# Performance work log

Hardware: AMD Instinct MI355X
Metric: run time of the kernel (lower is better)

## Reference

```python
import jax, jax.numpy as jnp
import numpy as np

E4M3_MAX = 448.0
IGNORE = -1000.0
ROTARY_BASE = 10000.0


def quant_dequant_e4m3(w):
    """Emulate per-tensor FP8 E4M3 quantize->dequantize (3 mantissa bits, max 448)."""
    amax = jnp.max(jnp.abs(w))
    scale = E4M3_MAX / jnp.maximum(amax, 1e-12)
    v = w * scale
    a = jnp.abs(v)
    # exponent clipped to E4M3 range (min normal exp -6, max 8)
    e = jnp.clip(jnp.floor(jnp.log2(jnp.maximum(a, 1e-30))), -6.0, 8.0)
    step = jnp.exp2(e - 3.0)  # 3 mantissa bits
    q = jnp.clip(jnp.round(v / step) * step, -E4M3_MAX, E4M3_MAX)
    return (q / scale).astype(w.dtype)


def rotary_sin_cos(rotary_dim, n_ctx):
    pos = jnp.arange(n_ctx, dtype=jnp.float32)
    dim = jnp.arange(rotary_dim // 2, dtype=jnp.float32)
    inv_freq = ROTARY_BASE ** (-dim / (rotary_dim / 2))
    ang = pos[:, None] * inv_freq[None, :]            # [n_ctx, rotary_dim//2]
    ang = jnp.concatenate([ang, ang], axis=-1)        # [n_ctx, rotary_dim]
    return jnp.sin(ang), jnp.cos(ang)


def apply_rotary(x, sin, cos, rotary_dim):
    # x: [B, S, H, Dh]; rotate first rotary_dim dims with rotate-half convention
    S = x.shape[1]
    x_rot, x_pass = x[..., :rotary_dim], x[..., rotary_dim:]
    half = rotary_dim // 2
    x_flip = jnp.concatenate([-x_rot[..., half:], x_rot[..., :half]], axis=-1)
    c = cos[:S][None, :, None, :]
    s = sin[:S][None, :, None, :]
    out = x_rot * c + x_flip * s
    return jnp.concatenate([out, x_pass], axis=-1) if rotary_dim < x.shape[-1] else out


def setup_inputs() -> dict:
    key = jax.random.key(0)
    ks = jax.random.split(key, 8)
    B, S, D, H, Dh = 2, 2048, 1024, 16, 64
    return {
        "query_input": jax.random.normal(ks[0], (B, S, D), jnp.float32),
        "key_input": jax.random.normal(ks[1], (B, S, D), jnp.float32),
        "value_input": jax.random.normal(ks[2], (B, S, D), jnp.float32),
        "W_Q": jax.random.normal(ks[3], (H, D, Dh), jnp.float32) * 0.02,
        "W_K": jax.random.normal(ks[4], (H, D, Dh), jnp.float32) * 0.02,
        "W_V": jax.random.normal(ks[5], (H, D, Dh), jnp.float32) * 0.02,
        "W_O": jax.random.normal(ks[6], (H, Dh, D), jnp.float32) * 0.02,
        "b_Q": jnp.zeros((H, Dh), jnp.float32),
        "b_K": jnp.zeros((H, Dh), jnp.float32),
        "b_V": jnp.zeros((H, Dh), jnp.float32),
        "b_O": jnp.zeros((D,), jnp.float32),
    }


def reference(query_input, key_input, value_input, W_Q, W_K, W_V, W_O, b_Q, b_K, b_V, b_O):
    B, S, D = query_input.shape
    H, _, Dh = W_Q.shape
    rotary_dim = Dh
    attn_scale = jnp.sqrt(jnp.asarray(Dh, jnp.float32))

    # FP8-quantized QKV weights/biases (E4M3 quant-dequant emulation)
    Wq = quant_dequant_e4m3(W_Q)
    Wk = quant_dequant_e4m3(W_K)
    Wv = quant_dequant_e4m3(W_V)
    bq = quant_dequant_e4m3(b_Q)
    bk = quant_dequant_e4m3(b_K)
    bv = quant_dequant_e4m3(b_V)

    q = jnp.einsum("bsd,hde->bshe", query_input, Wq) + bq  # [B,S,H,Dh]
    k = jnp.einsum("bsd,hde->bshe", key_input, Wk) + bk
    v = jnp.einsum("bsd,hde->bshe", value_input, Wv) + bv

    sin, cos = rotary_sin_cos(rotary_dim, S)
    q = apply_rotary(q, sin, cos, rotary_dim)
    k = apply_rotary(k, sin, cos, rotary_dim)

    scores = jnp.einsum("bqhe,bkhe->bhqk", q, k) / attn_scale  # [B,H,S,S]
    causal = jnp.tril(jnp.ones((S, S), bool))
    scores = jnp.where(causal[None, None], scores, IGNORE)
    pattern = jax.nn.softmax(scores, axis=-1)

    z = jnp.einsum("bhqk,bkhe->bqhe", pattern, v)             # [B,S,H,Dh]
    out = jnp.einsum("bqhe,hed->bqd", z, W_O) + b_O           # [B,S,D]
    return out
```

## Files before the change

### kernel.cpp

```cpp
#include <hip/hip_runtime.h>
#include <math.h>


typedef __attribute__((ext_vector_type(8))) short bf16x8;
typedef __attribute__((ext_vector_type(16))) float f32x16;
typedef __attribute__((ext_vector_type(4))) float f32x4;
typedef __attribute__((ext_vector_type(4))) float f4;

#define E4M3_MAX 448.0f

__device__ inline float bf2f(ushort u) { return __uint_as_float(((unsigned)u) << 16); }
__device__ inline ushort f2bf(float f) {
  unsigned u = __float_as_uint(f);
  return (ushort)((u + 0x7FFF + ((u >> 16) & 1)) >> 16);
}
__device__ inline unsigned pack2bf(float a, float b) {
  unsigned ua = __float_as_uint(a), ub = __float_as_uint(b);
  return ((ua + 0x8000u) >> 16) | ((ub + 0x8000u) & 0xFFFF0000u);
}

__device__ __forceinline__ void gll16(const ushort* g, ushort* l) {
  __builtin_amdgcn_global_load_lds(
      (const __attribute__((address_space(1))) unsigned int*)g,
      (__attribute__((address_space(3))) unsigned int*)l, 16, 0, 0);
}

__global__ void zero16_kernel(float* p) {
  if (threadIdx.x < 16) p[threadIdx.x] = 0.0f;
}

__global__ __launch_bounds__(256) void amax6_kernel(const float* __restrict__ p0,
                                                    const float* __restrict__ p1,
                                                    const float* __restrict__ p2,
                                                    const float* __restrict__ p3,
                                                    const float* __restrict__ p4,
                                                    const float* __restrict__ p5,
                                                    float* __restrict__ amax) {
  int y = blockIdx.y;
  const float* src = (y == 0) ? p0 : (y == 1) ? p1 : (y == 2) ? p2 : (y == 3) ? p3 : (y == 4) ? p4 : p5;
  int n = (y < 3) ? 1048576 : 1024;
  float m = 0.0f;
  int stride = gridDim.x * 256;
  for (int i = blockIdx.x * 256 + threadIdx.x; i < n; i += stride)
    m = fmaxf(m, fabsf(src[i]));
  #pragma unroll
  for (int off = 32; off > 0; off >>= 1)
    m = fmaxf(m, __shfl_xor(m, off));
  __shared__ float wred[4];
  if ((threadIdx.x & 63) == 0) wred[threadIdx.x >> 6] = m;
  __syncthreads();
  if (threadIdx.x == 0) {
    m = fmaxf(fmaxf(wred[0], wred[1]), fmaxf(wred[2], wred[3]));
    atomicMax((unsigned int*)(amax + y), __float_as_uint(m));
  }
}

__device__ inline float qdq_qval(float w, float amax) {
  float scale = E4M3_MAX / fmaxf(amax, 1e-12f);
  float v = w * scale;
  float a = fmaxf(fabsf(v), 1e-30f);
  int ex;
  (void)frexpf(a, &ex);
  float e = fminf(fmaxf((float)(ex - 1), -6.0f), 8.0f);
  float step = exp2f(e - 3.0f);
  float q = rintf(v / step) * step;
  return fminf(fmaxf(q, -E4M3_MAX), E4M3_MAX);
}

__global__ void qvec3_kernel(const float* __restrict__ b0, const float* __restrict__ b1,
                             const float* __restrict__ b2, const float* __restrict__ amax,
                             float* __restrict__ o0, float* __restrict__ o1,
                             float* __restrict__ o2) {
  int y = blockIdx.y;
  const float* b = (y == 0) ? b0 : (y == 1) ? b1 : b2;
  float* o = (y == 0) ? o0 : (y == 1) ? o1 : o2;
  float am = amax[3 + y];
  int idx = blockIdx.x * blockDim.x + threadIdx.x;
  if (idx < 1024) {
    float q = qdq_qval(b[idx], am);
    o[idx] = q * (fmaxf(am, 1e-12f) * (1.0f / E4M3_MAX));
  }
}

__global__ __launch_bounds__(256) void quant_repack_bt3(const float* __restrict__ W0,
                                                        const float* __restrict__ W1,
                                                        const float* __restrict__ W2,
                                                        const float* __restrict__ amaxp,
                                                        ushort* __restrict__ o0,
                                                        ushort* __restrict__ o1,
                                                        ushort* __restrict__ o2) {
  int z = blockIdx.z;
  const float* W = (z == 0) ? W0 : (z == 1) ? W1 : W2;
  ushort* Bt = (z == 0) ? o0 : (z == 1) ? o1 : o2;
  float amax = amaxp[z];
  __shared__ float tile[64][65];
  int d0 = blockIdx.x * 64, hh = blockIdx.y;
  int tid = threadIdx.x;
  int e = tid & 63, dd = tid >> 6;
  #pragma unroll
  for (int p = 0; p < 16; p++)
    tile[dd + p * 4][e] = W[(size_t)hh * 65536 + (size_t)(d0 + dd + p * 4) * 64 + e];
  __syncthreads();
  int d = tid & 63, ee = tid >> 6;
  #pragma unroll
  for (int p = 0; p < 16; p++) {
    int e2 = ee + p * 4;
    Bt[(size_t)(hh * 64 + e2) * 1024 + d0 + d] = f2bf(qdq_qval(tile[d][e2], amax));
  }
}

__global__ __launch_bounds__(256) void wo_trans(const float* __restrict__ W,
                                               ushort* __restrict__ Bt) {
  __shared__ float tile[64][65];
  int d0 = blockIdx.x * 64, he0 = blockIdx.y * 64;
  int tid = threadIdx.x;
  int dcol = tid & 63, hr = tid >> 6;
  #pragma unroll
  for (int p = 0; p < 16; p++)
    tile[hr + p * 4][dcol] = W[(size_t)(he0 + hr + p * 4) * 1024 + d0 + dcol];
  __syncthreads();
  int hcol = tid & 63, dr = tid >> 6;
  #pragma unroll
  for (int p = 0; p < 16; p++)
    Bt[(size_t)(d0 + dr + p * 4) * 1024 + he0 + hcol] = f2bf(tile[hcol][dr + p * 4]);
}

__global__ __launch_bounds__(256) void cvt3_kernel(const float* __restrict__ i0,
                                                   const float* __restrict__ i1,
                                                   const float* __restrict__ i2,
                                                   ushort* __restrict__ o0,
                                                   ushort* __restrict__ o1,
                                                   ushort* __restrict__ o2) {
  int y = blockIdx.y;
  const float* in = (y == 0) ? i0 : (y == 1) ? i1 : i2;
  ushort* out = (y == 0) ? o0 : (y == 1) ? o1 : o2;
  int i = blockIdx.x * 256 + threadIdx.x;
  f4 v = *(const f4*)(in + (size_t)i * 4);
  uint2 o;
  o.x = (unsigned)f2bf(v[0]) | ((unsigned)f2bf(v[1]) << 16);
  o.y = (unsigned)f2bf(v[2]) | ((unsigned)f2bf(v[3]) << 16);
  *(uint2*)(out + (size_t)i * 4) = o;
}

template <int QUANT, int TN>
__device__ __forceinline__ void gemm_body(const ushort* __restrict__ A,
                                          const ushort* __restrict__ Bt,
                                          const float* __restrict__ bias, float s_inv,
                                          ushort* __restrict__ outb, float* __restrict__ outf,
                                          int bx, int by, ushort* As, ushort* Bs) {
  const int K = 1024, N = 1024;
  const int JF = TN / 32;
  int tid = threadIdx.x;
  int w = tid >> 6, lane = tid & 63, quad = lane >> 4, l16 = lane & 15;
  int wm = w & 1, wn = w >> 1;
  int row0 = by * 128, col0 = bx * TN;
  f32x4 acc[4][4] = {};

  for (int k0 = 0; k0 < K; k0 += 32) {
    __syncthreads();
    {
      int u = tid;
      gll16(&A[(size_t)(row0 + (u >> 2)) * K + k0 + (u & 3) * 8], &As[u * 8]);
      u = tid + 256;
      gll16(&A[(size_t)(row0 + (u >> 2)) * K + k0 + (u & 3) * 8], &As[u * 8]);
      u = tid;
      gll16(&Bt[(size_t)(col0 + (u >> 2)) * K + k0 + (u & 3) * 8], &Bs[u * 8]);
      if (TN == 128) {
        u = tid + 256;
        gll16(&Bt[(size_t)(col0 + (u >> 2)) * K + k0 + (u & 3) * 8], &Bs[u * 8]);
      }
    }
    __syncthreads();
    bf16x8 af[4], bfr[JF];
    #pragma unroll
    for (int i = 0; i < 4; i++)
      af[i] = *(const bf16x8*)&As[(wm * 64 + i * 16 + l16) * 32 + quad * 8];
    #pragma unroll
    for (int j = 0; j < JF; j++)
      bfr[j] = *(const bf16x8*)&Bs[(wn * (TN / 2) + j * 16 + l16) * 32 + quad * 8];
    #pragma unroll
    for (int i = 0; i < 4; i++)
      #pragma unroll
      for (int j = 0; j < JF; j++)
        acc[i][j] = __builtin_amdgcn_mfma_f32_16x16x32_bf16(af[i], bfr[j], acc[i][j], 0, 0, 0);
  }

  #pragma unroll
  for (int j = 0; j < JF; j++) {
    int col = col0 + wn * (TN / 2) + j * 16 + l16;
    float bv = bias[col];
    #pragma unroll
    for (int i = 0; i < 4; i++) {
      int row = row0 + wm * 64 + i * 16 + quad * 4;
      #pragma unroll
      for (int r = 0; r < 4; r++) {
        float v = acc[i][j][r] * s_inv + bv;
        if (QUANT) outb[(size_t)(row + r) * N + col] = f2bf(v);
        else       outf[(size_t)(row + r) * N + col] = v;
      }
    }
  }
}

__global__ __launch_bounds__(256) void gemm3_qkv(const ushort* __restrict__ xq,
                                                 const ushort* __restrict__ xk,
                                                 const ushort* __restrict__ xv,
                                                 const ushort* __restrict__ wq,
                                                 const ushort* __restrict__ wk,
                                                 const ushort* __restrict__ wv,
                                                 const float* __restrict__ bq,
                                                 const float* __restrict__ bk,
                                                 const float* __restrict__ bv,
                                                 const float* __restrict__ amax,
                                                 ushort* __restrict__ oq,
                                                 ushort* __restrict__ ok,
                                                 ushort* __restrict__ ov) {
  __shared__ ushort As[4096], Bs[4096];
  int z = blockIdx.z;
  const ushort* A  = (z == 0) ? xq : (z == 1) ? xk : xv;
  const ushort* Bt = (z == 0) ? wq : (z == 1) ? wk : wv;
  const float* bias = (z == 0) ? bq : (z == 1) ? bk : bv;
  ushort* out = (z == 0) ? oq : (z == 1) ? ok : ov;
  float s_inv = fmaxf(amax[z], 1e-12f) * (1.0f / E4M3_MAX);
  gemm_body<1, 128>(A, Bt, bias, s_inv, out, nullptr, blockIdx.x, blockIdx.y, As, Bs);
}

__global__ __launch_bounds__(256) void gemm_wo(const ushort* __restrict__ A,
                                               const ushort* __restrict__ Bt,
                                               const float* __restrict__ bias,
                                               float* __restrict__ out) {
  __shared__ ushort As[4096], Bs[2048];
  gemm_body<0, 64>(A, Bt, bias, 1.0f, nullptr, out, blockIdx.x, blockIdx.y, As, Bs);
}

__global__ __launch_bounds__(256) void rotary_bf(ushort* qb, ushort* kb) {
  int bs = blockIdx.x;
  int s = bs & 2047;
  int tid = threadIdx.x;
  int e = tid & 63, w = tid >> 6;
  int j = e & 31;
  float inv_freq = exp2f((float)j * (-13.287712379549449f / 32.0f));
  float ang = (float)s * inv_freq;
  float c = cosf(ang), sn = sinf(ang);
  float sgn = (e < 32) ? -1.0f : 1.0f;
  size_t base = (size_t)bs * 1024;
  #pragma unroll
  for (int i = 0; i < 4; i++) {
    int h = w + i * 4;
    size_t idx = base + (size_t)h * 64 + e;
    float x = bf2f(qb[idx]);
    float xp = __shfl_xor(x, 32);
    qb[idx] = f2bf(x * c + sgn * xp * sn);
    float y = bf2f(kb[idx]);
    float yp = __shfl_xor(y, 32);
    kb[idx] = f2bf(y * c + sgn * yp * sn);
  }
}

__global__ __launch_bounds__(256) void v_trans(const ushort* __restrict__ v,
                                              ushort* __restrict__ vT) {
  __shared__ ushort tile[64][72];
  int s0 = blockIdx.x * 64, h = blockIdx.y, b = blockIdx.z;
  int tid = threadIdx.x;
  int e = tid & 63, sr = tid >> 6;
  #pragma unroll
  for (int p = 0; p < 16; p++)
    tile[sr + p * 4][e] = v[(size_t)(b * 2048 + s0 + sr + p * 4) * 1024 + h * 64 + e];
  __syncthreads();
  int sc = tid & 63, er = tid >> 6;
  #pragma unroll
  for (int p = 0; p < 16; p++)
    vT[(size_t)((b * 16 + h) * 64 + er + p * 4) * 2048 + s0 + sc] = tile[sc][er + p * 4];
}

__global__ __launch_bounds__(256, 2) void flash_mfma4(const ushort* __restrict__ qb,
                                                      const ushort* __restrict__ kb,
                                                      const ushort* __restrict__ vT,
                                                      ushort* __restrict__ zb) {
  int qt = (int)gridDim.x - 1 - (int)blockIdx.x;
  int h = blockIdx.y, b = blockIdx.z;
  int tid = threadIdx.x;
  int w = tid >> 6, lane = tid & 63, h2 = lane >> 5, l31 = lane & 31;
  __shared__ ushort sbuf[8192 + 9216];
  ushort* Ks = sbuf;
  ushort* Vs = sbuf + 4096;
  ushort* P2 = sbuf + 8192;

  const int q0 = qt * 128;
  const int qg = q0 + w * 32 + l31;
  const int qrow = w * 32 + l31;
  size_t qbase = ((size_t)(b * 2048 + qg)) * 1024 + (size_t)h * 64;
  bf16x8 qf[4];
  #pragma unroll
  for (int ck = 0; ck < 4; ck++)
    qf[ck] = *(const bf16x8*)&qb[qbase + ck * 16 + h2 * 8];

  f32x16 accO[2] = {};
  float mrun = -INFINITY, lrun = 0.0f;
  const float CE = 0.125f;

  const int u0 = tid, u1 = tid + 256;
  const int r0 = u0 >> 3, c0 = u0 & 7, r1 = u1 >> 3, c1 = u1 & 7;
  const int sw0 = (c0 ^ (r0 & 7)) * 8, sw1 = (c1 ^ (r1 & 7)) * 8;
  const ushort* ksrc0 = kb + ((size_t)(b * 2048 + r0)) * 1024 + (size_t)h * 64 + c0 * 8;
  const ushort* ksrc1 = kb + ((size_t)(b * 2048 + r1)) * 1024 + (size_t)h * 64 + c1 * 8;
  const ushort* vsrc0 = vT + ((size_t)((b * 16 + h) * 64 + r0)) * 2048 + c0 * 8;
  const ushort* vsrc1 = vT + ((size_t)((b * 16 + h) * 64 + r1)) * 2048 + c1 * 8;

  int ktmax = 2 * qt + 1;
  uint4 kc0 = *(const uint4*)ksrc0;
  uint4 kc1 = *(const uint4*)ksrc1;
  uint4 vc0 = *(const uint4*)vsrc0;
  uint4 vc1 = *(const uint4*)vsrc1;

  for (int kt = 0; kt <= ktmax; kt++) {
    __syncthreads();
    *(uint4*)&Ks[r0 * 64 + sw0] = kc0;
    *(uint4*)&Ks[r1 * 64 + sw1] = kc1;
    *(uint4*)&Vs[r0 * 64 + sw0] = vc0;
    *(uint4*)&Vs[r1 * 64 + sw1] = vc1;
    __syncthreads();
    if (kt < ktmax) {
      kc0 = *(const uint4*)(ksrc0 + (size_t)(kt + 1) * 65536);
      kc1 = *(const uint4*)(ksrc1 + (size_t)(kt + 1) * 65536);
      vc0 = *(const uint4*)(vsrc0 + (kt + 1) * 64);
      vc1 = *(const uint4*)(vsrc1 + (kt + 1) * 64);
    }

    bool active = (kt * 64 <= q0 + w * 32 + 31);
    if (active) {
      f32x16 sc[2] = {};
      #pragma unroll
      for (int mf = 0; mf < 2; mf++) {
        int row = mf * 32 + l31;
        int s8 = row & 7;
        #pragma unroll
        for (int ck = 0; ck < 4; ck++) {
          bf16x8 ka = *(const bf16x8*)&Ks[row * 64 + (((2 * ck + h2) ^ s8) * 8)];
          sc[mf] = __builtin_amdgcn_mfma_f32_32x32x16_bf16(ka, qf[ck], sc[mf], 0, 0, 0);
        }
      }

      if (kt * 64 + 63 > q0 + w * 32) {
        #pragma unroll
        for (int mf = 0; mf < 2; mf++)
          #pragma unroll
          for (int i = 0; i < 16; i++) {
            int kv = kt * 64 + mf * 32 + (i & 3) + 8 * (i >> 2) + 4 * h2;
            sc[mf][i] = (kv > qg) ? -8000.0f : sc[mf][i];
          }
      }

      float tm = sc[0][0];
      #pragma unroll
      for (int i = 1; i < 16; i++) tm = fmaxf(tm, sc[0][i]);
      #pragma unroll
      for (int i = 0; i < 16; i++) tm = fmaxf(tm, sc[1][i]);
      tm = fmaxf(tm, __shfl_xor(tm, 32));
      float mnew = fmaxf(mrun, tm);
      float alpha = __expf((mrun - mnew) * CE);
      float p[2][16];
      float rs = 0.0f;
      #pragma unroll
      for (int mf = 0; mf < 2; mf++)
        #pragma unroll
        for (int i = 0; i < 16; i++) {
          float pv = __expf((sc[mf][i] - mnew) * CE);
          p[mf][i] = pv;
          rs += pv;
        }
      rs += __shfl_xor(rs, 32);
      lrun = lrun * alpha + rs;
      mrun = mnew;
      #pragma unroll
      for (int mf = 0; mf < 2; mf++)
        #pragma unroll
        for (int i = 0; i < 16; i++) accO[mf][i] *= alpha;

      #pragma unroll
      for (int mf = 0; mf < 2; mf++)
        #pragma unroll
        for (int m = 0; m < 4; m++) {
          uint2 w2;
          w2.x = pack2bf(p[mf][4 * m + 0], p[mf][4 * m + 1]);
          w2.y = pack2bf(p[mf][4 * m + 2], p[mf][4 * m + 3]);
          *(uint2*)&P2[qrow * 72 + 32 * mf + 8 * m + 4 * h2] = w2;
        }
    }
    __syncthreads();
    if (active) {
      #pragma unroll
      for (int ck = 0; ck < 4; ck++) {
        bf16x8 pB = *(const bf16x8*)&P2[qrow * 72 + ck * 16 + h2 * 8];
        #pragma unroll
        for (int mf = 0; mf < 2; mf++) {
          int row = mf * 32 + l31;
          bf16x8 va = *(const bf16x8*)&Vs[row * 64 + (((2 * ck + h2) ^ (row & 7)) * 8)];
          accO[mf] = __builtin_amdgcn_mfma_f32_32x32x16_bf16(va, pB, accO[mf], 0, 0, 0);
        }
      }
    }
  }

  float inv = 1.0f / lrun;
  __syncthreads();
  ushort* Osb = P2;
  #pragma unroll
  for (int mf = 0; mf < 2; mf++)
    #pragma unroll
    for (int m = 0; m < 4; m++) {
      int e0 = 32 * mf + 8 * m + 4 * h2;
      float a0 = accO[mf][4 * m + 0] * inv, a1 = accO[mf][4 * m + 1] * inv;
      float a2 = accO[mf][4 * m + 2] * inv, a3 = accO[mf][4 * m + 3] * inv;
      *(unsigned*)&Osb[qrow * 72 + e0] = pack2bf(a0, a1);
      *(unsigned*)&Osb[qrow * 72 + e0 + 2] = pack2bf(a2, a3);
    }
  __syncthreads();
  size_t obase = ((size_t)(b * 2048 + q0)) * 1024 + (size_t)h * 64;
  #pragma unroll
  for (int i = 0; i < 4; i++) {
    int u = tid + i * 256;
    int r = u >> 3, blk = u & 7;
    *(uint4*)&zb[obase + (size_t)r * 1024 + blk * 8] = *(const uint4*)&Osb[r * 72 + blk * 8];
  }
}

extern "C" void kernel_launch(void* const* d_in, const int* in_sizes, int n_in,
                              void* d_out, int out_size, void* d_ws, size_t ws_size,
                              hipStream_t stream) {
  const float* Xq  = (const float*)d_in[0];
  const float* Xk  = (const float*)d_in[1];
  const float* Xv  = (const float*)d_in[2];
  const float* W_Q = (const float*)d_in[3];
  const float* W_K = (const float*)d_in[4];
  const float* W_V = (const float*)d_in[5];
  const float* W_O = (const float*)d_in[6];
  const float* b_Q = (const float*)d_in[7];
  const float* b_K = (const float*)d_in[8];
  const float* b_V = (const float*)d_in[9];
  const float* b_O = (const float*)d_in[10];
  float* out = (float*)d_out;

  char* base = (char*)d_ws;
  float*  amax = (float*)(base + 0);
  float*  bq   = (float*)(base + 4096);
  float*  bk   = (float*)(base + 8192);
  float*  bv   = (float*)(base + 12288);
  ushort* wq   = (ushort*)(base + 16384);
  ushort* wk   = (ushort*)(base + 16384 + 2097152);
  ushort* wv   = (ushort*)(base + 16384 + 2u * 2097152);
  ushort* woT  = (ushort*)(base + 16384 + 3u * 2097152);
  ushort* xq   = (ushort*)(base + 8404992);
  ushort* xk   = (ushort*)(base + 16793600);
  ushort* xv   = (ushort*)(base + 25182208);
  ushort* qbf  = (ushort*)(base + 33570816);
  ushort* kbf  = (ushort*)(base + 41959424);
  ushort* vbf  = (ushort*)(base + 50348032);
  ushort* vT   = xq;
  ushort* zbf  = xk;

  zero16_kernel<<<1, 64, 0, stream>>>(amax);
  dim3 agrid(64, 6);
  amax6_kernel<<<agrid, 256, 0, stream>>>(W_Q, W_K, W_V, b_Q, b_K, b_V, amax);

  dim3 rgrid(16, 16, 3);
  quant_repack_bt3<<<rgrid, 256, 0, stream>>>(W_Q, W_K, W_V, amax, wq, wk, wv);
  dim3 qvgrid(4, 3);
  qvec3_kernel<<<qvgrid, 256, 0, stream>>>(b_Q, b_K, b_V, amax, bq, bk, bv);
  dim3 wgrid(16, 16);
  wo_trans<<<wgrid, 256, 0, stream>>>(W_O, woT);
  dim3 cgrid(4096, 3);
  cvt3_kernel<<<cgrid, 256, 0, stream>>>(Xq, Xk, Xv, xq, xk, xv);

  dim3 g3(8, 32, 3);
  gemm3_qkv<<<g3, 256, 0, stream>>>(xq, xk, xv, wq, wk, wv, bq, bk, bv, amax,
                                    qbf, kbf, vbf);

  rotary_bf<<<4096, 256, 0, stream>>>(qbf, kbf);

  dim3 vgrid(32, 16, 2);
  v_trans<<<vgrid, 256, 0, stream>>>(vbf, vT);

  dim3 fgrid(16, 16, 2);
  flash_mfma4<<<fgrid, 256, 0, stream>>>(qbf, kbf, vT, zbf);

  dim3 wog(16, 32);
  gemm_wo<<<wog, 256, 0, stream>>>(zbf, woT, b_O, out);
}
```

Measured before the change: 275.1 us.

## Split flash attention KV range across two wave groups with final merge

The flash attention kernel now runs 512 threads per block. Two groups of four waves each take half of the causal key range for the same 128-query tile, and the partial outputs plus running max and sum are merged through shared memory at the end. The barrier between the P write and the PV matmul is also dropped, since each wave reads only its own P rows. This adds parallelism per query tile and shortens the serial KV loop, at the cost of doubled LDS use, a merge step and possible occupancy limits.

```diff
diff --git a/kernel.cpp b/kernel.cpp
--- a/kernel.cpp
+++ b/kernel.cpp
@@ -273,18 +273,21 @@
     vT[(size_t)((b * 16 + h) * 64 + er + p * 4) * 2048 + s0 + sc] = tile[sc][er + p * 4];
 }
 
-__global__ __launch_bounds__(256, 2) void flash_mfma4(const ushort* __restrict__ qb,
+__global__ __launch_bounds__(512, 4) void flash_mfma5(const ushort* __restrict__ qb,
                                                       const ushort* __restrict__ kb,
                                                       const ushort* __restrict__ vT,
                                                       ushort* __restrict__ zb) {
   int qt = (int)gridDim.x - 1 - (int)blockIdx.x;
   int h = blockIdx.y, b = blockIdx.z;
   int tid = threadIdx.x;
-  int w = tid >> 6, lane = tid & 63, h2 = lane >> 5, l31 = lane & 31;
-  __shared__ ushort sbuf[8192 + 9216];
-  ushort* Ks = sbuf;
-  ushort* Vs = sbuf + 4096;
-  ushort* P2 = sbuf + 8192;
+  int w8 = tid >> 6;
+  int g = w8 >> 2;
+  int w = w8 & 3;
+  int lane = tid & 63, h2 = lane >> 5, l31 = lane & 31;
+  __shared__ ushort sbuf[16384 + 18432];
+  ushort* Ks = sbuf + g * 4096;
+  ushort* Vs = sbuf + 8192 + g * 4096;
+  ushort* P2 = sbuf + 16384 + g * 9216;
 
   const int q0 = qt * 128;
   const int qg = q0 + w * 32 + l31;
@@ -299,32 +302,36 @@
   float mrun = -INFINITY, lrun = 0.0f;
   const float CE = 0.125f;
 
-  const int u0 = tid, u1 = tid + 256;
+  const int nt = qt + 1;
+  const int kt0 = g * nt;
+
+  const int ts = tid & 255;
+  const int u0 = ts, u1 = ts + 256;
   const int r0 = u0 >> 3, c0 = u0 & 7, r1 = u1 >> 3, c1 = u1 & 7;
   const int sw0 = (c0 ^ (r0 & 7)) * 8, sw1 = (c1 ^ (r1 & 7)) * 8;
-  const ushort* ksrc0 = kb + ((size_t)(b * 2048 + r0)) * 1024 + (size_t)h * 64 + c0 * 8;
-  const ushort* ksrc1 = kb + ((size_t)(b * 2048 + r1)) * 1024 + (size_t)h * 64 + c1 * 8;
-  const ushort* vsrc0 = vT + ((size_t)((b * 16 + h) * 64 + r0)) * 2048 + c0 * 8;
-  const ushort* vsrc1 = vT + ((size_t)((b * 16 + h) * 64 + r1)) * 2048 + c1 * 8;
-
-  int ktmax = 2 * qt + 1;
+  const ushort* ksrc0 = kb + ((size_t)(b * 2048 + kt0 * 64 + r0)) * 1024 + (size_t)h * 64 + c0 * 8;
+  const ushort* ksrc1 = kb + ((size_t)(b * 2048 + kt0 * 64 + r1)) * 1024 + (size_t)h * 64 + c1 * 8;
+  const ushort* vsrc0 = vT + ((size_t)((b * 16 + h) * 64 + r0)) * 2048 + kt0 * 64 + c0 * 8;
+  const ushort* vsrc1 = vT + ((size_t)((b * 16 + h) * 64 + r1)) * 2048 + kt0 * 64 + c1 * 8;
+
   uint4 kc0 = *(const uint4*)ksrc0;
   uint4 kc1 = *(const uint4*)ksrc1;
   uint4 vc0 = *(const uint4*)vsrc0;
   uint4 vc1 = *(const uint4*)vsrc1;
 
-  for (int kt = 0; kt <= ktmax; kt++) {
+  for (int t = 0; t < nt; t++) {
+    int kt = kt0 + t;
     __syncthreads();
     *(uint4*)&Ks[r0 * 64 + sw0] = kc0;
     *(uint4*)&Ks[r1 * 64 + sw1] = kc1;
     *(uint4*)&Vs[r0 * 64 + sw0] = vc0;
     *(uint4*)&Vs[r1 * 64 + sw1] = vc1;
     __syncthreads();
-    if (kt < ktmax) {
-      kc0 = *(const uint4*)(ksrc0 + (size_t)(kt + 1) * 65536);
-      kc1 = *(const uint4*)(ksrc1 + (size_t)(kt + 1) * 65536);
-      vc0 = *(const uint4*)(vsrc0 + (kt + 1) * 64);
-      vc1 = *(const uint4*)(vsrc1 + (kt + 1) * 64);
+    if (t + 1 < nt) {
+      kc0 = *(const uint4*)(ksrc0 + (size_t)(t + 1) * 65536);
+      kc1 = *(const uint4*)(ksrc1 + (size_t)(t + 1) * 65536);
+      vc0 = *(const uint4*)(vsrc0 + (t + 1) * 64);
+      vc1 = *(const uint4*)(vsrc1 + (t + 1) * 64);
     }
 
     bool active = (kt * 64 <= q0 + w * 32 + 31);
@@ -386,9 +393,7 @@
           w2.y = pack2bf(p[mf][4 * m + 2], p[mf][4 * m + 3]);
           *(uint2*)&P2[qrow * 72 + 32 * mf + 8 * m + 4 * h2] = w2;
         }
-    }
-    __syncthreads();
-    if (active) {
+
       #pragma unroll
       for (int ck = 0; ck < 4; ck++) {
         bf16x8 pB = *(const bf16x8*)&P2[qrow * 72 + ck * 16 + h2 * 8];
@@ -402,24 +407,42 @@
     }
   }
 
-  float inv = 1.0f / lrun;
-  __syncthreads();
-  ushort* Osb = P2;
-  #pragma unroll
-  for (int mf = 0; mf < 2; mf++)
-    #pragma unroll
-    for (int m = 0; m < 4; m++) {
-      int e0 = 32 * mf + 8 * m + 4 * h2;
-      float a0 = accO[mf][4 * m + 0] * inv, a1 = accO[mf][4 * m + 1] * inv;
-      float a2 = accO[mf][4 * m + 2] * inv, a3 = accO[mf][4 * m + 3] * inv;
-      *(unsigned*)&Osb[qrow * 72 + e0] = pack2bf(a0, a1);
-      *(unsigned*)&Osb[qrow * 72 + e0 + 2] = pack2bf(a2, a3);
-    }
+  __syncthreads();
+  float* mbuf = (float*)sbuf;
+  int midx = (w * 64 + lane) * 35;
+  if (g == 1) {
+    #pragma unroll
+    for (int i = 0; i < 16; i++) mbuf[midx + i] = accO[0][i];
+    #pragma unroll
+    for (int i = 0; i < 16; i++) mbuf[midx + 16 + i] = accO[1][i];
+    mbuf[midx + 32] = mrun;
+    mbuf[midx + 33] = lrun;
+  }
+  __syncthreads();
+  ushort* Osb = sbuf + 16384 + 9216;
+  if (g == 0) {
+    float m1 = mbuf[midx + 32], l1 = mbuf[midx + 33];
+    float mn = fmaxf(mrun, m1);
+    float a0 = __expf((mrun - mn) * CE), a1 = __expf((m1 - mn) * CE);
+    float linv = 1.0f / (lrun * a0 + l1 * a1);
+    #pragma unroll
+    for (int mf = 0; mf < 2; mf++)
+      #pragma unroll
+      for (int m = 0; m < 4; m++) {
+        int e0 = 32 * mf + 8 * m + 4 * h2;
+        float o0 = (accO[mf][4 * m + 0] * a0 + mbuf[midx + 16 * mf + 4 * m + 0] * a1) * linv;
+        float o1 = (accO[mf][4 * m + 1] * a0 + mbuf[midx + 16 * mf + 4 * m + 1] * a1) * linv;
+        float o2 = (accO[mf][4 * m + 2] * a0 + mbuf[midx + 16 * mf + 4 * m + 2] * a1) * linv;
+        float o3 = (accO[mf][4 * m + 3] * a0 + mbuf[midx + 16 * mf + 4 * m + 3] * a1) * linv;
+        *(unsigned*)&Osb[qrow * 72 + e0] = pack2bf(o0, o1);
+        *(unsigned*)&Osb[qrow * 72 + e0 + 2] = pack2bf(o2, o3);
+      }
+  }
   __syncthreads();
   size_t obase = ((size_t)(b * 2048 + q0)) * 1024 + (size_t)h * 64;
   #pragma unroll
-  for (int i = 0; i < 4; i++) {
-    int u = tid + i * 256;
+  for (int i = 0; i < 2; i++) {
+    int u = tid + i * 512;
     int r = u >> 3, blk = u & 7;
     *(uint4*)&zb[obase + (size_t)r * 1024 + blk * 8] = *(const uint4*)&Osb[r * 72 + blk * 8];
   }
@@ -479,10 +502,10 @@
   rotary_bf<<<4096, 256, 0, stream>>>(qbf, kbf);
 
   dim3 vgrid(32, 16, 2);
-  v_trans<<<vgrid, 256, 0, stream>>>(vbf, vT);
+  v_trans<<<vgrid, 16 * 16, 0, stream>>>(vbf, vT);
 
   dim3 fgrid(16, 16, 2);
-  flash_mfma4<<<fgrid, 256, 0, stream>>>(qbf, kbf, vT, zbf);
+  flash_mfma5<<<fgrid, 512, 0, stream>>>(qbf, kbf, vT, zbf);
 
   dim3 wog(16, 32);
   gemm_wo<<<wog, 256, 0, stream>>>(zbf, woT, b_O, out);
```

New measurement: 277.3 us. Within noise of the previous version (+0.8%).
